# Performance work log

Hardware: AMD Instinct MI355X
Metric: run time of the kernel (lower is better)

Reference implementation:

```python
import jax, jax.numpy as jnp
import numpy as np

A = 0.7071067811865476  # sqrt(2)/2
B_ = 1.0 - A
KH = KW = 3
K2 = 9
STRIDE = 1
PAD = 1
DIL = 1


def setup_inputs() -> dict:
    key = jax.random.key(0)
    k1, k2, k3, k4 = jax.random.split(key, 4)
    Bn, Cin, H, W = 4, 256, 64, 64
    Cout = 256
    x = jax.random.normal(k1, (Bn, Cin, H, W), dtype=jnp.float32)
    offset = jax.random.normal(k2, (Bn, 2 * K2, H, W), dtype=jnp.float32)
    mask = jax.random.uniform(k3, (Bn, K2, H, W), dtype=jnp.float32)
    stdv = 1.0 / np.sqrt(Cin * KH * KW)
    weight = jax.random.uniform(k4, (Cout, Cin, KH, KW), dtype=jnp.float32,
                                minval=-stdv, maxval=stdv)
    bias = jnp.zeros((Cout,), dtype=jnp.float32)
    return {"input": x, "offset": offset, "mask": mask, "weight": weight, "bias": bias}


def _weight_circle(weight):
    # Blend 3x3 corner taps along the diagonal "circle", as in DCNv2_Circle.forward.
    O, C = weight.shape[0], weight.shape[1]
    w = weight.reshape(O, C, K2)
    w0 = A * (A * w[:, :, 0] + B_ * w[:, :, 1]) + B_ * (A * w[:, :, 3] + B_ * w[:, :, 4])
    w2 = A * (B_ * w[:, :, 1] + A * w[:, :, 2]) + B_ * (B_ * w[:, :, 4] + A * w[:, :, 5])
    w6 = B_ * (A * w[:, :, 3] + B_ * w[:, :, 4]) + A * (A * w[:, :, 6] + B_ * w[:, :, 7])
    w8 = B_ * (B_ * w[:, :, 4] + A * w[:, :, 5]) + A * (B_ * w[:, :, 7] + A * w[:, :, 8])
    return jnp.stack([w0, w[:, :, 1], w2, w[:, :, 3], w[:, :, 4],
                      w[:, :, 5], w6, w[:, :, 7], w8], axis=-1)  # [O, C, 9]


def _dcn_v2(x, offset, mask, w_flat, bias):
    Bn, C, H, W = x.shape
    Ho = (H + 2 * PAD - DIL * (KH - 1) - 1) // STRIDE + 1
    Wo = (W + 2 * PAD - DIL * (KW - 1) - 1) // STRIDE + 1
    # Base sampling grid per kernel tap k: [K2, Ho, Wo]
    ki, kj = jnp.meshgrid(jnp.arange(KH), jnp.arange(KW), indexing="ij")
    ki = ki.reshape(K2).astype(jnp.float32)
    kj = kj.reshape(K2).astype(jnp.float32)
    oy = (jnp.arange(Ho, dtype=jnp.float32) * STRIDE - PAD)
    ox = (jnp.arange(Wo, dtype=jnp.float32) * STRIDE - PAD)
    base_y = oy[None, :, None] + DIL * ki[:, None, None]  # [K2, Ho, 1]
    base_x = ox[None, None, :] + DIL * kj[:, None, None]  # [K2, 1, Wo]
    # Offsets: channel 2k is dy, 2k+1 is dx (DCNv2 layout).
    off = offset.reshape(Bn, K2, 2, Ho, Wo)
    y = base_y[None] + off[:, :, 0]  # [B, K2, Ho, Wo]
    x_ = base_x[None] + off[:, :, 1]
    y0 = jnp.floor(y)
    x0 = jnp.floor(x_)
    ly = y - y0
    lx = x_ - x0
    y0i = y0.astype(jnp.int32)
    x0i = x0.astype(jnp.int32)
    flat = x.reshape(Bn, C, H * W)

    def gather(yi, xi):
        valid = (yi >= 0) & (yi < H) & (xi >= 0) & (xi < W)
        idx = jnp.clip(yi, 0, H - 1) * W + jnp.clip(xi, 0, W - 1)  # [B,K2,Ho,Wo]
        v = jax.vmap(lambda f, i: f[:, i.reshape(-1)])(flat, idx)  # [B,C,K2*Ho*Wo]
        v = v.reshape(Bn, C, K2, Ho, Wo)
        return v * valid[:, None].astype(v.dtype)

    hy = 1.0 - ly
    hx = 1.0 - lx
    # corner weights broadcast over channel dim
    sampled = (gather(y0i, x0i) * (hy * hx)[:, None]
               + gather(y0i, x0i + 1) * (hy * lx)[:, None]
               + gather(y0i + 1, x0i) * (ly * hx)[:, None]
               + gather(y0i + 1, x0i + 1) * (ly * lx)[:, None])  # [B,C,K2,Ho,Wo]
    sampled = sampled * mask[:, None]  # modulation
    out = jnp.einsum("bckhw,ock->bohw", sampled, w_flat)
    return out + bias[None, :, None, None]


def reference(input, offset, mask, weight, bias):
    w_flat = _weight_circle(weight)
    return _dcn_v2(input, offset, mask, w_flat, bias)
```

## Files before the change

### kernel.cpp

```cpp
#include <hip/hip_runtime.h>

typedef __bf16 bf16x8 __attribute__((ext_vector_type(8)));
typedef float f32x4 __attribute__((ext_vector_type(4)));

#define HH 64
#define WW 64
#define HW 4096
#define COUT 256
#define BSTRIDE 296
#define NROWS 12
#define XROW 65
#define XS_OFF 37888

__device__ __forceinline__ void bar_sync() {
    asm volatile("s_waitcnt lgkmcnt(0)" ::: "memory");
    __builtin_amdgcn_s_barrier();
    asm volatile("" ::: "memory");
}

__global__ __launch_bounds__(256) void prep_weights(const float* __restrict__ weight,
                                                    __bf16* __restrict__ wp) {
    const int t = blockIdx.x * 256 + threadIdx.x;
    const int lane = t & 63;
    const int tm   = (t >> 6) & 15;
    const int cg   = (t >> 10) & 7;
    const int tap  = t >> 13;
    const int rr = lane & 15, q = lane >> 4;
    const int o  = tm * 16 + rr;
    const int c0 = cg * 32 + q * 8;
    const float* wb = weight + ((size_t)o * 256 + c0) * 9;
    const float Af = 0.70710678118654752f;
    const float Bf = 1.0f - Af;
    bf16x8 v;
    #pragma unroll
    for (int j = 0; j < 8; ++j) {
        const float* w = wb + j * 9;
        float r;
        switch (tap) {
            case 0:  r = Af*(Af*w[0]+Bf*w[1]) + Bf*(Af*w[3]+Bf*w[4]); break;
            case 1:  r = w[1]; break;
            case 2:  r = Af*(Bf*w[1]+Af*w[2]) + Bf*(Bf*w[4]+Af*w[5]); break;
            case 3:  r = w[3]; break;
            case 4:  r = w[4]; break;
            case 5:  r = w[5]; break;
            case 6:  r = Bf*(Af*w[3]+Bf*w[4]) + Af*(Af*w[6]+Bf*w[7]); break;
            case 7:  r = w[7]; break;
            default: r = Bf*(Bf*w[4]+Af*w[5]) + Af*(Bf*w[7]+Af*w[8]); break;
        }
        v[j] = (__bf16)r;
    }
    const int ksg = cg * 9 + tap;
    *(bf16x8*)&wp[(size_t)(((ksg * 16 + tm) << 6) | lane) << 3] = v;
}

__global__ __launch_bounds__(512, 2) void dcn_main(
        const float* __restrict__ x, const float* __restrict__ off,
        const float* __restrict__ msk, const __bf16* __restrict__ wp,
        const float* __restrict__ bias, float* __restrict__ out) {
    __shared__ char smem[65536];
    __bf16* Xs = (__bf16*)(smem + XS_OFF);
    char* BsB  = smem;
    const char* XsB = (const char*)smem + XS_OFF;

    const int tid  = threadIdx.x;
    const int wv   = tid >> 6;
    const int lane = tid & 63;
    const int q    = lane >> 4, rr = lane & 15;
    const int px   = lane;

    const int bid = blockIdx.x;
    const int xcd = bid & 7;
    const int b   = xcd >> 1;
    const int h   = ((xcd & 1) << 5) | (bid >> 3);

    const int rowbase = min(max(h - 5, 0), HH - NROWS);
    const float* xb = x + (size_t)b * 256 * HW;

    int SGk[3], GOFF[3], XA[3];
    #pragma unroll
    for (int k = 0; k < 3; ++k) {
        int slot = k * 512 + tid;
        int sg   = slot / 768;
        int rem  = slot - sg * 768;
        int row  = rem >> 6, spx = rem & 63;
        SGk[k]  = sg;
        GOFF[k] = (rowbase + row) * 64 + spx;
        XA[k]   = ((sg * NROWS + row) * XROW + spx) << 3;
    }

    float W00[3], W01[3], W10[3], W11[3];
    int AY0[3], AY1[3], DXO[3], COLB[3], GP[3];
    bool UV[3];
    #pragma unroll
    for (int k = 0; k < 3; ++k) {
        int c = (k < 2) ? (wv + 8 * k) : ((wv >= 6) ? wv + 10 : -1);
        UV[k] = (c >= 0);
        if (UV[k]) {
            int sg = c / 9, tap = c % 9;
            int ki = tap / 3, kj = tap - 3 * ki;
            const float* offp = off + (size_t)b * 18 * HW + h * 64 + px;
            float dy = offp[(2 * tap) * HW];
            float dx = offp[(2 * tap + 1) * HW];
            float mv = msk[(size_t)b * 9 * HW + (size_t)tap * HW + h * 64 + px];
            float py  = (float)(h - 1 + ki) + dy;
            float pxf = (float)(px - 1 + kj) + dx;
            float y0f = floorf(py), x0f = floorf(pxf);
            float ly = py - y0f, lx = pxf - x0f;
            float hy = 1.0f - ly, hx = 1.0f - lx;
            int y0 = (int)y0f, x0 = (int)x0f;
            int y1 = y0 + 1, x1 = x0 + 1;
            bool vy0 = (y0 >= 0) && (y0 < HH), vy1 = (y1 >= 0) && (y1 < HH);
            bool vx0 = (x0 >= 0) && (x0 < WW), vx1 = (x1 >= 0) && (x1 < WW);
            int cy0 = min(max(y0, 0), HH - 1), cy1 = min(max(y1, 0), HH - 1);
            int cx0 = min(max(x0, 0), WW - 1), cx1 = min(max(x1, 0), WW - 1);
            W00[k] = (vy0 && vx0) ? hy * hx * mv : 0.0f;
            W01[k] = (vy0 && vx1) ? hy * lx * mv : 0.0f;
            W10[k] = (vy1 && vx0) ? ly * hx * mv : 0.0f;
            W11[k] = (vy1 && vx1) ? ly * lx * mv : 0.0f;
            int ry0 = min(max(cy0 - rowbase, 0), NROWS - 1);
            int ry1 = min(max(cy1 - rowbase, 0), NROWS - 1);
            bool useG = (vy0 && (cy0 < rowbase || cy0 > rowbase + NROWS - 1))
                     || (vy1 && (cy1 < rowbase || cy1 > rowbase + NROWS - 1));
            AY0[k]  = ((sg * NROWS + ry0) * XROW + cx0) * 16;
            AY1[k]  = ((sg * NROWS + ry1) * XROW + cx0) * 16;
            DXO[k]  = (cx1 - cx0) * 16;
            COLB[k] = (tap * 32 + sg * 8) * 2;
            GP[k]   = cy0 | (cy1 << 6) | (cx0 << 12) | (cx1 << 18) | (sg << 24)
                    | (useG ? (1u << 31) : 0);
        }
    }

    f32x4 acc[4][4];
    #pragma unroll
    for (int i = 0; i < 4; ++i)
        #pragma unroll
        for (int n = 0; n < 4; ++n)
            acc[i][n] = (f32x4)0.0f;

    const int tm0   = (wv & 3) * 4;
    const int klbeg = (wv & 4) ? 5 : 0;
    const int nkl   = (wv & 4) ? 4 : 5;

    float R[3][8];
    #pragma unroll
    for (int k = 0; k < 3; ++k) {
        const float* p = xb + (size_t)(SGk[k] * 8) * HW + GOFF[k];
        #pragma unroll
        for (int j = 0; j < 8; ++j) R[k][j] = p[j * HW];
    }

    #pragma unroll 1
    for (int s = 0; s < 16; ++s) {
        const int cg = s >> 1, half = s & 1;
        bar_sync();
        #pragma unroll
        for (int k = 0; k < 3; ++k) {
            bf16x8 v;
            #pragma unroll
            for (int j = 0; j < 8; ++j) v[j] = (__bf16)R[k][j];
            *(bf16x8*)&Xs[XA[k]] = v;
        }
        if (s < 15) {
            const int s1 = s + 1;
            const int cbase = (s1 >> 1) * 32 + (s1 & 1) * 16;
            #pragma unroll
            for (int k = 0; k < 3; ++k) {
                const float* p = xb + (size_t)(cbase + SGk[k] * 8) * HW + GOFF[k];
                #pragma unroll
                for (int j = 0; j < 8; ++j) R[k][j] = p[j * HW];
            }
        }
        bar_sync();
        #pragma unroll
        for (int k = 0; k < 3; ++k) {
            if (UV[k]) {
                bf16x8 c00 = *(const bf16x8*)(XsB + AY0[k]);
                bf16x8 c01 = *(const bf16x8*)(XsB + AY0[k] + DXO[k]);
                bf16x8 c10 = *(const bf16x8*)(XsB + AY1[k]);
                bf16x8 c11 = *(const bf16x8*)(XsB + AY1[k] + DXO[k]);
                float w0 = W00[k], w1 = W01[k], w2 = W10[k], w3 = W11[k];
                bf16x8 res;
                #pragma unroll
                for (int j = 0; j < 8; ++j) {
                    float v = w0 * (float)c00[j] + w1 * (float)c01[j]
                            + w2 * (float)c10[j] + w3 * (float)c11[j];
                    res[j] = (__bf16)v;
                }
                int gp = GP[k];
                if (gp < 0) {
                    int cy0 = gp & 63, cy1 = (gp >> 6) & 63;
                    int cx0 = (gp >> 12) & 63, cx1 = (gp >> 18) & 63;
                    int sg = (gp >> 24) & 3;
                    const float* xc = xb + (size_t)(cg * 32 + half * 16 + sg * 8) * HW;
                    int i00 = cy0 * 64 + cx0, i01 = cy0 * 64 + cx1;
                    int i10 = cy1 * 64 + cx0, i11 = cy1 * 64 + cx1;
                    #pragma unroll
                    for (int j = 0; j < 8; ++j) {
                        float v = w0 * xc[i00] + w1 * xc[i01]
                                + w2 * xc[i10] + w3 * xc[i11];
                        res[j] = (__bf16)v;
                        xc += HW;
                    }
                }
                *(bf16x8*)(BsB + px * 592 + COLB[k] + half * 32) = res;
            }
        }
        if (half) {
            bar_sync();
            const __bf16* ap = wp + ((size_t)((cg * 9 + klbeg) * 16 + tm0) * 64 + lane) * 8;
            bf16x8 a0 = *(const bf16x8*)ap;
            bf16x8 a1 = *(const bf16x8*)(ap + 512);
            bf16x8 a2 = *(const bf16x8*)(ap + 1024);
            bf16x8 a3 = *(const bf16x8*)(ap + 1536);
            int kc = (klbeg * 32 + q * 8) * 2;
            #pragma unroll 1
            for (int t = 0; t < nkl; ++t) {
                bf16x8 n0 = a0, n1 = a1, n2 = a2, n3 = a3;
                if (t + 1 < nkl) {
                    const __bf16* np = ap + 8192;
                    n0 = *(const bf16x8*)np;
                    n1 = *(const bf16x8*)(np + 512);
                    n2 = *(const bf16x8*)(np + 1024);
                    n3 = *(const bf16x8*)(np + 1536);
                }
                const char* bp = BsB + rr * 592 + kc;
                bf16x8 bb0 = *(const bf16x8*)(bp);
                bf16x8 bb1 = *(const bf16x8*)(bp + 16 * 592);
                bf16x8 bb2 = *(const bf16x8*)(bp + 32 * 592);
                bf16x8 bb3 = *(const bf16x8*)(bp + 48 * 592);
                acc[0][0] = __builtin_amdgcn_mfma_f32_16x16x32_bf16(a0, bb0, acc[0][0], 0, 0, 0);
                acc[1][0] = __builtin_amdgcn_mfma_f32_16x16x32_bf16(a1, bb0, acc[1][0], 0, 0, 0);
                acc[2][0] = __builtin_amdgcn_mfma_f32_16x16x32_bf16(a2, bb0, acc[2][0], 0, 0, 0);
                acc[3][0] = __builtin_amdgcn_mfma_f32_16x16x32_bf16(a3, bb0, acc[3][0], 0, 0, 0);
                acc[0][1] = __builtin_amdgcn_mfma_f32_16x16x32_bf16(a0, bb1, acc[0][1], 0, 0, 0);
                acc[1][1] = __builtin_amdgcn_mfma_f32_16x16x32_bf16(a1, bb1, acc[1][1], 0, 0, 0);
                acc[2][1] = __builtin_amdgcn_mfma_f32_16x16x32_bf16(a2, bb1, acc[2][1], 0, 0, 0);
                acc[3][1] = __builtin_amdgcn_mfma_f32_16x16x32_bf16(a3, bb1, acc[3][1], 0, 0, 0);
                acc[0][2] = __builtin_amdgcn_mfma_f32_16x16x32_bf16(a0, bb2, acc[0][2], 0, 0, 0);
                acc[1][2] = __builtin_amdgcn_mfma_f32_16x16x32_bf16(a1, bb2, acc[1][2], 0, 0, 0);
                acc[2][2] = __builtin_amdgcn_mfma_f32_16x16x32_bf16(a2, bb2, acc[2][2], 0, 0, 0);
                acc[3][2] = __builtin_amdgcn_mfma_f32_16x16x32_bf16(a3, bb2, acc[3][2], 0, 0, 0);
                acc[0][3] = __builtin_amdgcn_mfma_f32_16x16x32_bf16(a0, bb3, acc[0][3], 0, 0, 0);
                acc[1][3] = __builtin_amdgcn_mfma_f32_16x16x32_bf16(a1, bb3, acc[1][3], 0, 0, 0);
                acc[2][3] = __builtin_amdgcn_mfma_f32_16x16x32_bf16(a2, bb3, acc[2][3], 0, 0, 0);
                acc[3][3] = __builtin_amdgcn_mfma_f32_16x16x32_bf16(a3, bb3, acc[3][3], 0, 0, 0);
                ap += 8192;
                kc += 64;
                a0 = n0; a1 = n1; a2 = n2; a3 = n3;
            }
        }
    }

    float* scr = (float*)smem;
    bar_sync();
    if (wv >= 4) {
        const int base = (wv - 4) * 4096 + lane * 4;
        #pragma unroll
        for (int i = 0; i < 4; ++i)
            #pragma unroll
            for (int n = 0; n < 4; ++n)
                *(f32x4*)&scr[base + (i * 4 + n) * 256] = acc[i][n];
    }
    bar_sync();
    if (wv < 4) {
        const int mrow = wv * 64;
        const int base = wv * 4096 + lane * 4;
        #pragma unroll
        for (int i = 0; i < 4; ++i) {
            #pragma unroll
            for (int n = 0; n < 4; ++n) {
                f32x4 p = *(const f32x4*)&scr[base + (i * 4 + n) * 256];
                #pragma unroll
                for (int e = 0; e < 4; ++e) {
                    int m = mrow + i * 16 + q * 4 + e;
                    out[((size_t)b * COUT + m) * HW + h * 64 + n * 16 + rr]
                        = acc[i][n][e] + p[e] + bias[m];
                }
            }
        }
    }
}

extern "C" void kernel_launch(void* const* d_in, const int* in_sizes, int n_in,
                              void* d_out, int out_size, void* d_ws, size_t ws_size,
                              hipStream_t stream) {
    const float* x      = (const float*)d_in[0];
    const float* off    = (const float*)d_in[1];
    const float* msk    = (const float*)d_in[2];
    const float* weight = (const float*)d_in[3];
    const float* bias   = (const float*)d_in[4];
    float* out = (float*)d_out;

    __bf16* wp = (__bf16*)d_ws;

    prep_weights<<<288, 256, 0, stream>>>(weight, wp);
    dcn_main<<<256, 512, 0, stream>>>(x, off, msk, wp, bias, out);
}
```

Baseline: 125.1 us.

## Split each output row into two 32-column halves and coalesce weight prep loads

The main kernel now tiles each output row into two 32-pixel halves, doubling the grid to 512 blocks. Each block stages a smaller 12x40 input window in LDS, which shrinks shared memory and raises the occupancy target to 4 blocks per CU. Samples that fall outside the window take a global-memory fallback. Weight prep now gives each block one output channel, loads its weights coalesced through LDS, and writes the same packed layout. The trade-off is more redundant halo loads of the input and less MFMA work per block.

```diff
diff --git a/kernel.cpp b/kernel.cpp
--- a/kernel.cpp
+++ b/kernel.cpp
@@ -7,10 +7,11 @@
 #define WW 64
 #define HW 4096
 #define COUT 256
-#define BSTRIDE 296
 #define NROWS 12
-#define XROW 65
-#define XS_OFF 37888
+#define NCOLS 40
+#define XROW 41
+#define XS_OFF 18944
+#define SMEM_SZ 34688
 
 __device__ __forceinline__ void bar_sync() {
     asm volatile("s_waitcnt lgkmcnt(0)" ::: "memory");
@@ -20,44 +21,51 @@
 
 __global__ __launch_bounds__(256) void prep_weights(const float* __restrict__ weight,
                                                     __bf16* __restrict__ wp) {
-    const int t = blockIdx.x * 256 + threadIdx.x;
-    const int lane = t & 63;
-    const int tm   = (t >> 6) & 15;
-    const int cg   = (t >> 10) & 7;
-    const int tap  = t >> 13;
-    const int rr = lane & 15, q = lane >> 4;
-    const int o  = tm * 16 + rr;
-    const int c0 = cg * 32 + q * 8;
-    const float* wb = weight + ((size_t)o * 256 + c0) * 9;
+    __shared__ float ws[2304];
+    const int o = blockIdx.x;
+    const int tid = threadIdx.x;
+    const float4* src = (const float4*)(weight + (size_t)o * 2304);
+    float4* dst = (float4*)ws;
+    #pragma unroll
+    for (int i = 0; i < 3; ++i) {
+        int idx = i * 256 + tid;
+        if (idx < 576) dst[idx] = src[idx];
+    }
+    __syncthreads();
     const float Af = 0.70710678118654752f;
     const float Bf = 1.0f - Af;
-    bf16x8 v;
-    #pragma unroll
-    for (int j = 0; j < 8; ++j) {
-        const float* w = wb + j * 9;
-        float r;
-        switch (tap) {
-            case 0:  r = Af*(Af*w[0]+Bf*w[1]) + Bf*(Af*w[3]+Bf*w[4]); break;
-            case 1:  r = w[1]; break;
-            case 2:  r = Af*(Bf*w[1]+Af*w[2]) + Bf*(Bf*w[4]+Af*w[5]); break;
-            case 3:  r = w[3]; break;
-            case 4:  r = w[4]; break;
-            case 5:  r = w[5]; break;
-            case 6:  r = Bf*(Af*w[3]+Bf*w[4]) + Af*(Af*w[6]+Bf*w[7]); break;
-            case 7:  r = w[7]; break;
-            default: r = Bf*(Bf*w[4]+Af*w[5]) + Af*(Bf*w[7]+Af*w[8]); break;
-        }
-        v[j] = (__bf16)r;
-    }
-    const int ksg = cg * 9 + tap;
-    *(bf16x8*)&wp[(size_t)(((ksg * 16 + tm) << 6) | lane) << 3] = v;
+    const int tm = o >> 4, rr = o & 15;
+    for (int fid = tid; fid < 288; fid += 256) {
+        const int cgtap = fid >> 2, q = fid & 3;
+        const int cg = cgtap / 9, tap = cgtap - 9 * cg;
+        const int c0 = cg * 32 + q * 8;
+        bf16x8 v;
+        #pragma unroll
+        for (int j = 0; j < 8; ++j) {
+            const float* w = ws + (c0 + j) * 9;
+            float r;
+            switch (tap) {
+                case 0:  r = Af*(Af*w[0]+Bf*w[1]) + Bf*(Af*w[3]+Bf*w[4]); break;
+                case 1:  r = w[1]; break;
+                case 2:  r = Af*(Bf*w[1]+Af*w[2]) + Bf*(Bf*w[4]+Af*w[5]); break;
+                case 3:  r = w[3]; break;
+                case 4:  r = w[4]; break;
+                case 5:  r = w[5]; break;
+                case 6:  r = Bf*(Af*w[3]+Bf*w[4]) + Af*(Af*w[6]+Bf*w[7]); break;
+                case 7:  r = w[7]; break;
+                default: r = Bf*(Bf*w[4]+Af*w[5]) + Af*(Bf*w[7]+Af*w[8]); break;
+            }
+            v[j] = (__bf16)r;
+        }
+        *(bf16x8*)&wp[(size_t)(((cg * 9 + tap) * 16 + tm) * 64 + q * 16 + rr) << 3] = v;
+    }
 }
 
-__global__ __launch_bounds__(512, 2) void dcn_main(
+__global__ __launch_bounds__(512, 4) void dcn_main(
         const float* __restrict__ x, const float* __restrict__ off,
         const float* __restrict__ msk, const __bf16* __restrict__ wp,
         const float* __restrict__ bias, float* __restrict__ out) {
-    __shared__ char smem[65536];
+    __shared__ __align__(16) char smem[SMEM_SZ];
     __bf16* Xs = (__bf16*)(smem + XS_OFF);
     char* BsB  = smem;
     const char* XsB = (const char*)smem + XS_OFF;
@@ -66,44 +74,49 @@
     const int wv   = tid >> 6;
     const int lane = tid & 63;
     const int q    = lane >> 4, rr = lane & 15;
-    const int px   = lane;
+    const int px   = lane & 31;
+    const int side = lane >> 5;
 
     const int bid = blockIdx.x;
     const int xcd = bid & 7;
+    const int p   = bid >> 3;
     const int b   = xcd >> 1;
-    const int h   = ((xcd & 1) << 5) | (bid >> 3);
+    const int h   = ((xcd & 1) << 5) | (p & 31);
+    const int wb  = (p >> 5) << 5;
 
     const int rowbase = min(max(h - 5, 0), HH - NROWS);
+    const int colbase = min(max(wb - 6, 0), WW - NCOLS);
     const float* xb = x + (size_t)b * 256 * HW;
 
-    int SGk[3], GOFF[3], XA[3];
-    #pragma unroll
-    for (int k = 0; k < 3; ++k) {
+    int PXO[2], XA[2];
+    #pragma unroll
+    for (int k = 0; k < 2; ++k) {
         int slot = k * 512 + tid;
-        int sg   = slot / 768;
-        int rem  = slot - sg * 768;
-        int row  = rem >> 6, spx = rem & 63;
-        SGk[k]  = sg;
-        GOFF[k] = (rowbase + row) * 64 + spx;
-        XA[k]   = ((sg * NROWS + row) * XROW + spx) << 3;
-    }
-
-    float W00[3], W01[3], W10[3], W11[3];
-    int AY0[3], AY1[3], DXO[3], COLB[3], GP[3];
-    bool UV[3];
-    #pragma unroll
-    for (int k = 0; k < 3; ++k) {
-        int c = (k < 2) ? (wv + 8 * k) : ((wv >= 6) ? wv + 10 : -1);
-        UV[k] = (c >= 0);
-        if (UV[k]) {
-            int sg = c / 9, tap = c % 9;
+        if (slot < 960) {
+            int sg  = slot / 480;
+            int rem = slot - sg * 480;
+            int row = rem / 40, col = rem - row * 40;
+            PXO[k] = sg * 8 * HW + (rowbase + row) * 64 + (colbase + col);
+            XA[k]  = ((sg * NROWS + row) * XROW + col) << 3;
+        }
+    }
+    const bool st1 = (tid < 448);
+
+    const int nu = (wv == 7) ? 2 : 1;
+    float W00[2], W01[2], W10[2], W11[2];
+    int AY0[2], AY1[2], DXO[2], COLB[2], GP[2];
+    #pragma unroll
+    for (int k = 0; k < 2; ++k) {
+        if (k < nu) {
+            int c = (k == 0) ? (wv + 8 * side) : (16 + side);
+            int sg = c / 9, tap = c - 9 * sg;
             int ki = tap / 3, kj = tap - 3 * ki;
-            const float* offp = off + (size_t)b * 18 * HW + h * 64 + px;
+            const float* offp = off + (size_t)b * 18 * HW + h * 64 + wb + px;
             float dy = offp[(2 * tap) * HW];
             float dx = offp[(2 * tap + 1) * HW];
-            float mv = msk[(size_t)b * 9 * HW + (size_t)tap * HW + h * 64 + px];
+            float mv = msk[(size_t)b * 9 * HW + (size_t)tap * HW + h * 64 + wb + px];
             float py  = (float)(h - 1 + ki) + dy;
-            float pxf = (float)(px - 1 + kj) + dx;
+            float pxf = (float)(wb + px - 1 + kj) + dx;
             float y0f = floorf(py), x0f = floorf(pxf);
             float ly = py - y0f, lx = pxf - x0f;
             float hy = 1.0f - ly, hx = 1.0f - lx;
@@ -119,34 +132,44 @@
             W11[k] = (vy1 && vx1) ? ly * lx * mv : 0.0f;
             int ry0 = min(max(cy0 - rowbase, 0), NROWS - 1);
             int ry1 = min(max(cy1 - rowbase, 0), NROWS - 1);
-            bool useG = (vy0 && (cy0 < rowbase || cy0 > rowbase + NROWS - 1))
-                     || (vy1 && (cy1 < rowbase || cy1 > rowbase + NROWS - 1));
-            AY0[k]  = ((sg * NROWS + ry0) * XROW + cx0) * 16;
-            AY1[k]  = ((sg * NROWS + ry1) * XROW + cx0) * 16;
-            DXO[k]  = (cx1 - cx0) * 16;
+            int rx0 = min(max(cx0 - colbase, 0), NCOLS - 1);
+            int rx1 = min(max(cx1 - colbase, 0), NCOLS - 1);
+            bool in_r0 = (cy0 >= rowbase) && (cy0 < rowbase + NROWS);
+            bool in_r1 = (cy1 >= rowbase) && (cy1 < rowbase + NROWS);
+            bool in_c0 = (cx0 >= colbase) && (cx0 < colbase + NCOLS);
+            bool in_c1 = (cx1 >= colbase) && (cx1 < colbase + NCOLS);
+            bool useG = (vy0 && vx0 && !(in_r0 && in_c0))
+                     || (vy0 && vx1 && !(in_r0 && in_c1))
+                     || (vy1 && vx0 && !(in_r1 && in_c0))
+                     || (vy1 && vx1 && !(in_r1 && in_c1));
+            AY0[k]  = ((sg * NROWS + ry0) * XROW + rx0) * 16;
+            AY1[k]  = ((sg * NROWS + ry1) * XROW + rx0) * 16;
+            DXO[k]  = (rx1 - rx0) * 16;
             COLB[k] = (tap * 32 + sg * 8) * 2;
             GP[k]   = cy0 | (cy1 << 6) | (cx0 << 12) | (cx1 << 18) | (sg << 24)
                     | (useG ? (1u << 31) : 0);
         }
     }
 
-    f32x4 acc[4][4];
+    f32x4 acc[4][2];
     #pragma unroll
     for (int i = 0; i < 4; ++i)
         #pragma unroll
-        for (int n = 0; n < 4; ++n)
+        for (int n = 0; n < 2; ++n)
             acc[i][n] = (f32x4)0.0f;
 
     const int tm0   = (wv & 3) * 4;
     const int klbeg = (wv & 4) ? 5 : 0;
     const int nkl   = (wv & 4) ? 4 : 5;
 
-    float R[3][8];
-    #pragma unroll
-    for (int k = 0; k < 3; ++k) {
-        const float* p = xb + (size_t)(SGk[k] * 8) * HW + GOFF[k];
-        #pragma unroll
-        for (int j = 0; j < 8; ++j) R[k][j] = p[j * HW];
+    float R[2][8];
+    #pragma unroll
+    for (int k = 0; k < 2; ++k) {
+        if (k == 0 || st1) {
+            const float* pp = xb + PXO[k];
+            #pragma unroll
+            for (int j = 0; j < 8; ++j) R[k][j] = pp[j * HW];
+        }
     }
 
     #pragma unroll 1
@@ -154,26 +177,30 @@
         const int cg = s >> 1, half = s & 1;
         bar_sync();
         #pragma unroll
-        for (int k = 0; k < 3; ++k) {
-            bf16x8 v;
-            #pragma unroll
-            for (int j = 0; j < 8; ++j) v[j] = (__bf16)R[k][j];
-            *(bf16x8*)&Xs[XA[k]] = v;
+        for (int k = 0; k < 2; ++k) {
+            if (k == 0 || st1) {
+                bf16x8 v;
+                #pragma unroll
+                for (int j = 0; j < 8; ++j) v[j] = (__bf16)R[k][j];
+                *(bf16x8*)&Xs[XA[k]] = v;
+            }
         }
         if (s < 15) {
             const int s1 = s + 1;
             const int cbase = (s1 >> 1) * 32 + (s1 & 1) * 16;
             #pragma unroll
-            for (int k = 0; k < 3; ++k) {
-                const float* p = xb + (size_t)(cbase + SGk[k] * 8) * HW + GOFF[k];
-                #pragma unroll
-                for (int j = 0; j < 8; ++j) R[k][j] = p[j * HW];
+            for (int k = 0; k < 2; ++k) {
+                if (k == 0 || st1) {
+                    const float* pp = xb + (size_t)cbase * HW + PXO[k];
+                    #pragma unroll
+                    for (int j = 0; j < 8; ++j) R[k][j] = pp[j * HW];
+                }
             }
         }
         bar_sync();
         #pragma unroll
-        for (int k = 0; k < 3; ++k) {
-            if (UV[k]) {
+        for (int k = 0; k < 2; ++k) {
+            if (k < nu) {
                 bf16x8 c00 = *(const bf16x8*)(XsB + AY0[k]);
                 bf16x8 c01 = *(const bf16x8*)(XsB + AY0[k] + DXO[k]);
                 bf16x8 c10 = *(const bf16x8*)(XsB + AY1[k]);
@@ -226,8 +253,6 @@
                 const char* bp = BsB + rr * 592 + kc;
                 bf16x8 bb0 = *(const bf16x8*)(bp);
                 bf16x8 bb1 = *(const bf16x8*)(bp + 16 * 592);
-                bf16x8 bb2 = *(const bf16x8*)(bp + 32 * 592);
-                bf16x8 bb3 = *(const bf16x8*)(bp + 48 * 592);
                 acc[0][0] = __builtin_amdgcn_mfma_f32_16x16x32_bf16(a0, bb0, acc[0][0], 0, 0, 0);
                 acc[1][0] = __builtin_amdgcn_mfma_f32_16x16x32_bf16(a1, bb0, acc[1][0], 0, 0, 0);
                 acc[2][0] = __builtin_amdgcn_mfma_f32_16x16x32_bf16(a2, bb0, acc[2][0], 0, 0, 0);
@@ -236,14 +261,6 @@
                 acc[1][1] = __builtin_amdgcn_mfma_f32_16x16x32_bf16(a1, bb1, acc[1][1], 0, 0, 0);
                 acc[2][1] = __builtin_amdgcn_mfma_f32_16x16x32_bf16(a2, bb1, acc[2][1], 0, 0, 0);
                 acc[3][1] = __builtin_amdgcn_mfma_f32_16x16x32_bf16(a3, bb1, acc[3][1], 0, 0, 0);
-                acc[0][2] = __builtin_amdgcn_mfma_f32_16x16x32_bf16(a0, bb2, acc[0][2], 0, 0, 0);
-                acc[1][2] = __builtin_amdgcn_mfma_f32_16x16x32_bf16(a1, bb2, acc[1][2], 0, 0, 0);
-                acc[2][2] = __builtin_amdgcn_mfma_f32_16x16x32_bf16(a2, bb2, acc[2][2], 0, 0, 0);
-                acc[3][2] = __builtin_amdgcn_mfma_f32_16x16x32_bf16(a3, bb2, acc[3][2], 0, 0, 0);
-                acc[0][3] = __builtin_amdgcn_mfma_f32_16x16x32_bf16(a0, bb3, acc[0][3], 0, 0, 0);
-                acc[1][3] = __builtin_amdgcn_mfma_f32_16x16x32_bf16(a1, bb3, acc[1][3], 0, 0, 0);
-                acc[2][3] = __builtin_amdgcn_mfma_f32_16x16x32_bf16(a2, bb3, acc[2][3], 0, 0, 0);
-                acc[3][3] = __builtin_amdgcn_mfma_f32_16x16x32_bf16(a3, bb3, acc[3][3], 0, 0, 0);
                 ap += 8192;
                 kc += 64;
                 a0 = n0; a1 = n1; a2 = n2; a3 = n3;
@@ -254,27 +271,27 @@
     float* scr = (float*)smem;
     bar_sync();
     if (wv >= 4) {
-        const int base = (wv - 4) * 4096 + lane * 4;
+        const int base = (wv - 4) * 2048 + lane * 4;
         #pragma unroll
         for (int i = 0; i < 4; ++i)
             #pragma unroll
-            for (int n = 0; n < 4; ++n)
-                *(f32x4*)&scr[base + (i * 4 + n) * 256] = acc[i][n];
+            for (int n = 0; n < 2; ++n)
+                *(f32x4*)&scr[base + (i * 2 + n) * 256] = acc[i][n];
     }
     bar_sync();
     if (wv < 4) {
         const int mrow = wv * 64;
-        const int base = wv * 4096 + lane * 4;
+        const int base = wv * 2048 + lane * 4;
         #pragma unroll
         for (int i = 0; i < 4; ++i) {
             #pragma unroll
-            for (int n = 0; n < 4; ++n) {
-                f32x4 p = *(const f32x4*)&scr[base + (i * 4 + n) * 256];
+            for (int n = 0; n < 2; ++n) {
+                f32x4 pv = *(const f32x4*)&scr[base + (i * 2 + n) * 256];
                 #pragma unroll
                 for (int e = 0; e < 4; ++e) {
                     int m = mrow + i * 16 + q * 4 + e;
-                    out[((size_t)b * COUT + m) * HW + h * 64 + n * 16 + rr]
-                        = acc[i][n][e] + p[e] + bias[m];
+                    out[((size_t)b * COUT + m) * HW + h * 64 + wb + n * 16 + rr]
+                        = acc[i][n][e] + pv[e] + bias[m];
                 }
             }
         }
@@ -293,6 +310,6 @@
 
     __bf16* wp = (__bf16*)d_ws;
 
-    prep_weights<<<288, 256, 0, stream>>>(weight, wp);
-    dcn_main<<<256, 512, 0, stream>>>(x, off, msk, wp, bias, out);
+    prep_weights<<<256, 256, 0, stream>>>(weight, wp);
+    dcn_main<<<512, 512, 0, stream>>>(x, off, msk, wp, bias, out);
 }
```

Result: slower. 172.6 us (+37.9%).

## Pre-transpose input to bf16 channel-last and stream tiles via global_load_lds

Applied to the files above, without the earlier changes.

Adds a prep_x kernel that converts x from fp32 NCHW into a bf16 layout grouped by row and 16-channel slice, so each staged tile is contiguous. The main kernel then fills the LDS input tile with direct global-to-LDS async loads instead of register-staged fp32 loads plus conversion, removing the conversion work and one barrier per step. prep_weights is also restructured to stage each output channel's weights in shared memory. The cost is an extra kernel launch and a full extra pass over x to write the bf16 copy, and the LDS row padding is dropped, which may raise bank conflicts.

```diff
diff --git a/kernel.cpp b/kernel.cpp
--- a/kernel.cpp
+++ b/kernel.cpp
@@ -7,59 +7,101 @@
 #define WW 64
 #define HW 4096
 #define COUT 256
-#define BSTRIDE 296
 #define NROWS 12
-#define XROW 65
 #define XS_OFF 37888
+#define SMEM_SZ 65536
 
 __device__ __forceinline__ void bar_sync() {
     asm volatile("s_waitcnt lgkmcnt(0)" ::: "memory");
     __builtin_amdgcn_s_barrier();
     asm volatile("" ::: "memory");
 }
+__device__ __forceinline__ void bar_sync_vm() {
+    asm volatile("s_waitcnt vmcnt(0) lgkmcnt(0)" ::: "memory");
+    __builtin_amdgcn_s_barrier();
+    asm volatile("" ::: "memory");
+}
 
 __global__ __launch_bounds__(256) void prep_weights(const float* __restrict__ weight,
                                                     __bf16* __restrict__ wp) {
-    const int t = blockIdx.x * 256 + threadIdx.x;
-    const int lane = t & 63;
-    const int tm   = (t >> 6) & 15;
-    const int cg   = (t >> 10) & 7;
-    const int tap  = t >> 13;
-    const int rr = lane & 15, q = lane >> 4;
-    const int o  = tm * 16 + rr;
-    const int c0 = cg * 32 + q * 8;
-    const float* wb = weight + ((size_t)o * 256 + c0) * 9;
+    __shared__ float ws[2304];
+    const int o = blockIdx.x;
+    const int tid = threadIdx.x;
+    const float4* src = (const float4*)(weight + (size_t)o * 2304);
+    float4* dst = (float4*)ws;
+    #pragma unroll
+    for (int i = 0; i < 3; ++i) {
+        int idx = i * 256 + tid;
+        if (idx < 576) dst[idx] = src[idx];
+    }
+    __syncthreads();
     const float Af = 0.70710678118654752f;
     const float Bf = 1.0f - Af;
-    bf16x8 v;
-    #pragma unroll
-    for (int j = 0; j < 8; ++j) {
-        const float* w = wb + j * 9;
-        float r;
-        switch (tap) {
-            case 0:  r = Af*(Af*w[0]+Bf*w[1]) + Bf*(Af*w[3]+Bf*w[4]); break;
-            case 1:  r = w[1]; break;
-            case 2:  r = Af*(Bf*w[1]+Af*w[2]) + Bf*(Bf*w[4]+Af*w[5]); break;
-            case 3:  r = w[3]; break;
-            case 4:  r = w[4]; break;
-            case 5:  r = w[5]; break;
-            case 6:  r = Bf*(Af*w[3]+Bf*w[4]) + Af*(Af*w[6]+Bf*w[7]); break;
-            case 7:  r = w[7]; break;
-            default: r = Bf*(Bf*w[4]+Af*w[5]) + Af*(Bf*w[7]+Af*w[8]); break;
-        }
-        v[j] = (__bf16)r;
-    }
-    const int ksg = cg * 9 + tap;
-    *(bf16x8*)&wp[(size_t)(((ksg * 16 + tm) << 6) | lane) << 3] = v;
+    const int tm = o >> 4, rr = o & 15;
+    for (int fid = tid; fid < 288; fid += 256) {
+        const int cgtap = fid >> 2, q = fid & 3;
+        const int cg = cgtap / 9, tap = cgtap - 9 * cg;
+        const int c0 = cg * 32 + q * 8;
+        bf16x8 v;
+        #pragma unroll
+        for (int j = 0; j < 8; ++j) {
+            const float* w = ws + (c0 + j) * 9;
+            float r;
+            switch (tap) {
+                case 0:  r = Af*(Af*w[0]+Bf*w[1]) + Bf*(Af*w[3]+Bf*w[4]); break;
+                case 1:  r = w[1]; break;
+                case 2:  r = Af*(Bf*w[1]+Af*w[2]) + Bf*(Bf*w[4]+Af*w[5]); break;
+                case 3:  r = w[3]; break;
+                case 4:  r = w[4]; break;
+                case 5:  r = w[5]; break;
+                case 6:  r = Bf*(Af*w[3]+Bf*w[4]) + Af*(Af*w[6]+Bf*w[7]); break;
+                case 7:  r = w[7]; break;
+                default: r = Bf*(Bf*w[4]+Af*w[5]) + Af*(Bf*w[7]+Af*w[8]); break;
+            }
+            v[j] = (__bf16)r;
+        }
+        *(bf16x8*)&wp[(size_t)(((cg * 9 + tap) * 16 + tm) * 64 + q * 16 + rr) << 3] = v;
+    }
+}
+
+__global__ __launch_bounds__(256) void prep_x(const float* __restrict__ x,
+                                              __bf16* __restrict__ xs) {
+    __shared__ float lds[16384];
+    const int bh = blockIdx.x;
+    const int tid = threadIdx.x;
+    const int b = bh >> 6, h = bh & 63;
+    const int w4 = (tid & 15) * 4;
+    const int cb = tid >> 4;
+    #pragma unroll
+    for (int it = 0; it < 16; ++it) {
+        const int c = cb + it * 16;
+        float4 v = *(const float4*)(x + ((size_t)(b * 256 + c)) * HW + h * 64 + w4);
+        #pragma unroll
+        for (int e = 0; e < 4; ++e) {
+            int w = w4 + e;
+            lds[w * 256 + (c ^ (w & 31))] = ((const float*)&v)[e];
+        }
+    }
+    __syncthreads();
+    #pragma unroll
+    for (int it = 0; it < 8; ++it) {
+        const int u = it * 256 + tid;
+        const int gsg = u >> 6, w = u & 63;
+        bf16x8 v;
+        #pragma unroll
+        for (int c8 = 0; c8 < 8; ++c8)
+            v[c8] = (__bf16)lds[w * 256 + ((gsg * 8 + c8) ^ (w & 31))];
+        *(bf16x8*)&xs[(size_t)bh * 16384 + (size_t)u * 8] = v;
+    }
 }
 
 __global__ __launch_bounds__(512, 2) void dcn_main(
         const float* __restrict__ x, const float* __restrict__ off,
         const float* __restrict__ msk, const __bf16* __restrict__ wp,
-        const float* __restrict__ bias, float* __restrict__ out) {
-    __shared__ char smem[65536];
-    __bf16* Xs = (__bf16*)(smem + XS_OFF);
-    char* BsB  = smem;
+        const __bf16* __restrict__ xs, const float* __restrict__ bias,
+        float* __restrict__ out) {
+    __shared__ __align__(16) char smem[SMEM_SZ];
+    char* BsB = smem;
     const char* XsB = (const char*)smem + XS_OFF;
 
     const int tid  = threadIdx.x;
@@ -75,17 +117,15 @@
 
     const int rowbase = min(max(h - 5, 0), HH - NROWS);
     const float* xb = x + (size_t)b * 256 * HW;
-
-    int SGk[3], GOFF[3], XA[3];
+    const char* xsb = (const char*)xs;
+
+    size_t SB[3]; int XD[3];
     #pragma unroll
     for (int k = 0; k < 3; ++k) {
-        int slot = k * 512 + tid;
-        int sg   = slot / 768;
-        int rem  = slot - sg * 768;
-        int row  = rem >> 6, spx = rem & 63;
-        SGk[k]  = sg;
-        GOFF[k] = (rowbase + row) * 64 + spx;
-        XA[k]   = ((sg * NROWS + row) * XROW + spx) << 3;
+        int t = wv * 3 + k;
+        int row = t >> 1, sgh = t & 1;
+        SB[k] = (size_t)(b * 64 + rowbase + row) * 32768 + (size_t)(sgh * 1024 + lane * 16);
+        XD[k] = XS_OFF + row * 2048 + sgh * 1024;
     }
 
     float W00[3], W01[3], W10[3], W11[3];
@@ -121,8 +161,8 @@
             int ry1 = min(max(cy1 - rowbase, 0), NROWS - 1);
             bool useG = (vy0 && (cy0 < rowbase || cy0 > rowbase + NROWS - 1))
                      || (vy1 && (cy1 < rowbase || cy1 > rowbase + NROWS - 1));
-            AY0[k]  = ((sg * NROWS + ry0) * XROW + cx0) * 16;
-            AY1[k]  = ((sg * NROWS + ry1) * XROW + cx0) * 16;
+            AY0[k]  = ry0 * 2048 + sg * 1024 + cx0 * 16;
+            AY1[k]  = ry1 * 2048 + sg * 1024 + cx0 * 16;
             DXO[k]  = (cx1 - cx0) * 16;
             COLB[k] = (tap * 32 + sg * 8) * 2;
             GP[k]   = cy0 | (cy1 << 6) | (cx0 << 12) | (cx1 << 18) | (sg << 24)
@@ -141,36 +181,16 @@
     const int klbeg = (wv & 4) ? 5 : 0;
     const int nkl   = (wv & 4) ? 4 : 5;
 
-    float R[3][8];
-    #pragma unroll
-    for (int k = 0; k < 3; ++k) {
-        const float* p = xb + (size_t)(SGk[k] * 8) * HW + GOFF[k];
-        #pragma unroll
-        for (int j = 0; j < 8; ++j) R[k][j] = p[j * HW];
-    }
+    #pragma unroll
+    for (int k = 0; k < 3; ++k)
+        __builtin_amdgcn_global_load_lds(
+            (const __attribute__((address_space(1))) void*)(xsb + SB[k]),
+            (__attribute__((address_space(3))) void*)(smem + XD[k]), 16, 0, 0);
 
     #pragma unroll 1
     for (int s = 0; s < 16; ++s) {
         const int cg = s >> 1, half = s & 1;
-        bar_sync();
-        #pragma unroll
-        for (int k = 0; k < 3; ++k) {
-            bf16x8 v;
-            #pragma unroll
-            for (int j = 0; j < 8; ++j) v[j] = (__bf16)R[k][j];
-            *(bf16x8*)&Xs[XA[k]] = v;
-        }
-        if (s < 15) {
-            const int s1 = s + 1;
-            const int cbase = (s1 >> 1) * 32 + (s1 & 1) * 16;
-            #pragma unroll
-            for (int k = 0; k < 3; ++k) {
-                const float* p = xb + (size_t)(cbase + SGk[k] * 8) * HW + GOFF[k];
-                #pragma unroll
-                for (int j = 0; j < 8; ++j) R[k][j] = p[j * HW];
-            }
-        }
-        bar_sync();
+        bar_sync_vm();
         #pragma unroll
         for (int k = 0; k < 3; ++k) {
             if (UV[k]) {
@@ -205,8 +225,15 @@
                 *(bf16x8*)(BsB + px * 592 + COLB[k] + half * 32) = res;
             }
         }
+        bar_sync();
+        if (s < 15) {
+            #pragma unroll
+            for (int k = 0; k < 3; ++k)
+                __builtin_amdgcn_global_load_lds(
+                    (const __attribute__((address_space(1))) void*)(xsb + SB[k] + (size_t)(s + 1) * 2048),
+                    (__attribute__((address_space(3))) void*)(smem + XD[k]), 16, 0, 0);
+        }
         if (half) {
-            bar_sync();
             const __bf16* ap = wp + ((size_t)((cg * 9 + klbeg) * 16 + tm0) * 64 + lane) * 8;
             bf16x8 a0 = *(const bf16x8*)ap;
             bf16x8 a1 = *(const bf16x8*)(ap + 512);
@@ -292,7 +319,9 @@
     float* out = (float*)d_out;
 
     __bf16* wp = (__bf16*)d_ws;
-
-    prep_weights<<<288, 256, 0, stream>>>(weight, wp);
-    dcn_main<<<256, 512, 0, stream>>>(x, off, msk, wp, bias, out);
-}
+    __bf16* xs = (__bf16*)((char*)d_ws + 1179648);
+
+    prep_weights<<<256, 256, 0, stream>>>(weight, wp);
+    prep_x<<<256, 256, 0, stream>>>(x, xs);
+    dcn_main<<<256, 512, 0, stream>>>(x, off, msk, wp, xs, bias, out);
+}
```

Result: slower. 133.3 us (+6.6%).
